# Optimization experiments

Hardware: AMD Instinct MI355X
Metric: run time of the kernel (lower is better)

The kernel has to match this reference:

```python
import jax, jax.numpy as jnp
import numpy as np

B, N_MAX, D_MODEL, K_F, ROD_ID_DIM = 16384, 64, 256, 8, 8
BETA = 10000.0
PRECOMP = 64  # FourierFeatures precompute_limit
DISK_FEAT = 2 + 2 * K_F + 3 + ROD_ID_DIM   # 29
ROD_FEAT = 2 + 1 + 1 + 2 * 2 * K_F + ROD_ID_DIM  # 44


def fourier_table():
    # sin/cos interleaved as in torch: stack([sin,cos],-1).view(P, 2K)
    k = jnp.arange(K_F, dtype=jnp.float32)
    omega = BETA ** (-2.0 * k / (2.0 * K_F))
    idx = jnp.arange(PRECOMP, dtype=jnp.float32)
    oi = idx[:, None] * omega  # (P, K)
    return jnp.stack([jnp.sin(oi), jnp.cos(oi)], axis=-1).reshape(PRECOMP, 2 * K_F)


def setup_inputs() -> dict:
    key = jax.random.key(0)
    ks = jax.random.split(key, 8)
    state = jax.random.randint(ks[0], (B, N_MAX), 0, 3, dtype=jnp.int32)
    s = 0.02
    return {
        'state': state,
        'rod_id_embed': jax.random.normal(ks[1], (3, ROD_ID_DIM), jnp.float32),
        'disk_W': jax.random.normal(ks[2], (DISK_FEAT, D_MODEL), jnp.float32) * s,
        'disk_b': jax.random.normal(ks[3], (D_MODEL,), jnp.float32) * s,
        'rod_W': jax.random.normal(ks[4], (ROD_FEAT, D_MODEL), jnp.float32) * s,
        'rod_b': jax.random.normal(ks[5], (D_MODEL,), jnp.float32) * s,
        'null_fourier': jax.random.normal(ks[6], (2 * K_F,), jnp.float32) * s,
        'padding_embedding': jax.random.normal(ks[7], (D_MODEL,), jnp.float32) * s,
    }


def reference(state, rod_id_embed, disk_W, disk_b, rod_W, rod_b, null_fourier, padding_embedding):
    Bq, N = state.shape
    table = fourier_table()                      # (P, 2K)
    valid = state != -1                          # (B, N)
    lengths = valid.sum(axis=1)                  # (B,)
    state_safe = jnp.clip(state, 0, 2)

    # ---- vectorized _compute_state_info ----
    onehot = (state[:, None, :] == jnp.arange(3, dtype=state.dtype)[None, :, None]) & valid[:, None, :]  # (B,3,N)
    oh = onehot.astype(jnp.float32)
    counts = oh.sum(-1)                          # (B,3) disks per rod
    is_empty = counts == 0.0
    len_norm = counts / jnp.maximum(lengths, 1).astype(jnp.float32)[:, None]
    top_disk = jnp.argmax(onehot, axis=-1)       # min index on rod (top = smallest disk)
    bottom_disk = (N - 1) - jnp.argmax(onehot[:, :, ::-1], axis=-1)
    # per-disk: 'above' = # of smaller-index disks on same rod (exclusive prefix sum)
    cum = jnp.cumsum(oh, axis=-1) - oh           # (B,3,N)
    above = jnp.take_along_axis(cum, state_safe[:, None, :], axis=1)[:, 0, :]   # (B,N)
    height = jnp.take_along_axis(counts, state_safe, axis=1)                    # (B,N)
    vf = valid.astype(jnp.float32)
    is_top = (above == 0.0).astype(jnp.float32) * vf
    is_bottom = (above == height - 1.0).astype(jnp.float32) * vf
    depth_norm = jnp.where(height > 1.0, above / jnp.maximum(height - 1.0, 1.0), 0.0) * vf

    # ---- rod nodes (3) ----
    rod_type = jnp.broadcast_to(jnp.array([0.0, 1.0], jnp.float32), (Bq, 3, 2))
    top_f = table[top_disk]                      # (B,3,2K)
    bot_f = table[bottom_disk]
    emp = is_empty[:, :, None]
    top_f = jnp.where(emp, null_fourier, top_f)
    bot_f = jnp.where(emp, null_fourier, bot_f)
    rod_ids = jnp.broadcast_to(rod_id_embed[None], (Bq, 3, ROD_ID_DIM))
    rod_feats = jnp.concatenate([
        rod_type, len_norm[:, :, None], emp.astype(jnp.float32), top_f, bot_f, rod_ids], axis=-1)  # (B,3,44)
    rod_emb = jnp.einsum('brf,fd->brd', rod_feats, rod_W) + rod_b

    # ---- disk nodes (N) ----
    disk_type = jnp.broadcast_to(jnp.array([1.0, 0.0], jnp.float32), (Bq, N, 2))
    size_f = jnp.broadcast_to(table[:N][None], (Bq, N, 2 * K_F))
    rod_id_vec = rod_id_embed[state_safe]        # (B,N,rod_id_dim)
    disk_feats = jnp.concatenate([
        disk_type, size_f, depth_norm[:, :, None], is_top[:, :, None], is_bottom[:, :, None], rod_id_vec], axis=-1)  # (B,N,29)
    disk_emb = jnp.einsum('bnf,fd->bnd', disk_feats, disk_W) + disk_b
    disk_emb = jnp.where(valid[:, :, None], disk_emb, padding_embedding)

    return jnp.concatenate([rod_emb, disk_emb], axis=1)  # (B, 3+N, d_model)
```

## Files before the change

kernel.cpp:

```cpp
#include <hip/hip_runtime.h>

#define DM 256
#define NMAX 64

#define OFF_BASEROD 49152
#define OFF_RODTOP  49920
#define OFF_RODBOT  66560

typedef float vf4 __attribute__((ext_vector_type(4)));

static __device__ __forceinline__ vf4 ld4(const float* p) {
  return *reinterpret_cast<const vf4*>(p);
}
static __device__ __forceinline__ void st4_nt(float* p, vf4 v) {
  __builtin_nontemporal_store(v, reinterpret_cast<vf4*>(p));
}

__global__ void precomp_kernel(
    const float* __restrict__ rod_id_embed,
    const float* __restrict__ disk_W,
    const float* __restrict__ disk_b,
    const float* __restrict__ rod_W,
    const float* __restrict__ rod_b,
    const float* __restrict__ null_fourier,
    float* __restrict__ ws) {
  const int idx = blockIdx.x;
  const int d = threadIdx.x;

  float F[16];
  if (idx < 64) {
#pragma unroll
    for (int k = 0; k < 8; ++k) {
      float omega = powf(10000.0f, -(float)k * 0.125f);
      float a = (float)idx * omega;
      F[2 * k]     = sinf(a);
      F[2 * k + 1] = cosf(a);
    }
  } else {
#pragma unroll
    for (int k = 0; k < 16; ++k) F[k] = null_fourier[k];
  }

  float* bdc     = ws;
  float* baseRod = ws + OFF_BASEROD;
  float* rodTop  = ws + OFF_RODTOP;
  float* rodBot  = ws + OFF_RODBOT;

  float t = 0.f, bo = 0.f;
#pragma unroll
  for (int k = 0; k < 16; ++k) {
    t  += F[k] * rod_W[(4 + k) * DM + d];
    bo += F[k] * rod_W[(20 + k) * DM + d];
  }
  rodTop[idx * DM + d] = t;
  rodBot[idx * DM + d] = bo;

  if (idx < 64) {
    float base = disk_b[d] + disk_W[0 * DM + d];
#pragma unroll
    for (int k = 0; k < 16; ++k) base += F[k] * disk_W[(2 + k) * DM + d];
#pragma unroll
    for (int s = 0; s < 3; ++s) {
      float v = base;
#pragma unroll
      for (int j = 0; j < 8; ++j)
        v += rod_id_embed[s * 8 + j] * disk_W[(21 + j) * DM + d];
      bdc[(size_t)(s * 64 + idx) * DM + d] = v;
    }
  }
  if (idx < 3) {
    float br = rod_b[d] + rod_W[1 * DM + d];
#pragma unroll
    for (int j = 0; j < 8; ++j)
      br += rod_id_embed[idx * 8 + j] * rod_W[(36 + j) * DM + d];
    baseRod[idx * DM + d] = br;
  }
}

__launch_bounds__(256)
__global__ void enc_kernel(
    const int* __restrict__ state,
    const float* __restrict__ disk_W,
    const float* __restrict__ rod_W,
    const float* __restrict__ padding_embedding,
    const float* __restrict__ ws,
    float* __restrict__ out,
    int Btot) {
  const float* bdc     = ws;
  const float* baseRod = ws + OFF_BASEROD;
  const float* rodTop  = ws + OFF_RODTOP;
  const float* rodBot  = ws + OFF_RODBOT;

  const int w    = threadIdx.x >> 6;
  const int lane = threadIdx.x & 63;
  long b = (long)blockIdx.x * 4 + w;
  if (b >= Btot) b = Btot - 1;

  __shared__ vf4 meta_sh[4][64];
  __shared__ float lnorm_sh[4][3];
  __shared__ float emp_sh[4][3];
  __shared__ int   ti_sh[4][3];
  __shared__ int   bi_sh[4][3];

  const int s = state[b * NMAX + lane];
  const bool valid = (s >= 0);
  const int ss = s <= 0 ? 0 : (s >= 2 ? 2 : s);
  const unsigned long long m0 = __ballot(valid && s == 0);
  const unsigned long long m1 = __ballot(valid && s == 1);
  const unsigned long long m2 = __ballot(valid && s == 2);
  const unsigned long long vm = __ballot(valid);
  const unsigned long long mym = (ss == 0) ? m0 : ((ss == 1) ? m1 : m2);
  const int above  = __popcll(mym & ((1ull << lane) - 1ull));
  const int height = __popcll(mym);

  vf4 md;
  md.x = valid ? (float)(ss + 1) : 0.f;
  md.y = (valid && height > 1) ? (float)above / (float)(height - 1) : 0.f;
  md.z = (valid && above == 0) ? 1.f : 0.f;
  md.w = (valid && above == height - 1) ? 1.f : 0.f;
  meta_sh[w][lane] = md;

  if (lane < 3) {
    const unsigned long long m = (lane == 0) ? m0 : ((lane == 1) ? m1 : m2);
    const int cnt = __popcll(m);
    const int lengths = __popcll(vm);
    lnorm_sh[w][lane] = (float)cnt / (float)(lengths > 1 ? lengths : 1);
    emp_sh[w][lane]   = (cnt == 0) ? 1.f : 0.f;
    ti_sh[w][lane]    = cnt ? (int)__builtin_ctzll(m) : 64;
    bi_sh[w][lane]    = cnt ? 63 - (int)__builtin_clzll(m) : 64;
  }
  __syncthreads();

  const int c0 = lane * 4;
  const vf4 Wdep = ld4(disk_W + 18 * DM + c0);
  const vf4 Wt   = ld4(disk_W + 19 * DM + c0);
  const vf4 Wb   = ld4(disk_W + 20 * DM + c0);
  const vf4 pad  = ld4(padding_embedding + c0);
  const vf4 rW2  = ld4(rod_W + 2 * DM + c0);
  const vf4 rW3  = ld4(rod_W + 3 * DM + c0);

  float* outB = out + (size_t)b * 67 * DM;

#pragma unroll
  for (int r = 0; r < 3; ++r) {
    const float ln = lnorm_sh[w][r];
    const float em = emp_sh[w][r];
    const int ti = ti_sh[w][r];
    const int bi = bi_sh[w][r];
    vf4 v = ld4(baseRod + r * DM + c0);
    const vf4 tf = ld4(rodTop + (size_t)ti * DM + c0);
    const vf4 bf = ld4(rodBot + (size_t)bi * DM + c0);
    v += ln * rW2 + em * rW3 + tf + bf;
    st4_nt(outB + r * DM + c0, v);
  }

#pragma unroll 8
  for (int i = 0; i < 64; ++i) {
    const vf4 md2 = meta_sh[w][i];
    vf4 v;
    if (md2.x > 0.5f) {
      const int c = (int)md2.x - 1;
      const vf4 base = ld4(bdc + (size_t)(c * 64 + i) * DM + c0);
      v = base + md2.y * Wdep + md2.z * Wt + md2.w * Wb;
    } else {
      v = pad;
    }
    st4_nt(outB + (size_t)(3 + i) * DM + c0, v);
  }
}

extern "C" void kernel_launch(void* const* d_in, const int* in_sizes, int n_in,
                              void* d_out, int out_size, void* d_ws, size_t ws_size,
                              hipStream_t stream) {
  const int*   state             = (const int*)d_in[0];
  const float* rod_id_embed      = (const float*)d_in[1];
  const float* disk_W            = (const float*)d_in[2];
  const float* disk_b            = (const float*)d_in[3];
  const float* rod_W             = (const float*)d_in[4];
  const float* rod_b             = (const float*)d_in[5];
  const float* null_fourier      = (const float*)d_in[6];
  const float* padding_embedding = (const float*)d_in[7];
  float* ws  = (float*)d_ws;
  float* out = (float*)d_out;

  const int B = in_sizes[0] / NMAX;

  hipLaunchKernelGGL(precomp_kernel, dim3(65), dim3(256), 0, stream,
                     rod_id_embed, disk_W, disk_b, rod_W, rod_b, null_fourier, ws);
  hipLaunchKernelGGL(enc_kernel, dim3((B + 3) / 4), dim3(256), 0, stream,
                     state, disk_W, rod_W, padding_embedding, ws, out, B);
}
```

Before: 228.5 us.

## Stage per-disk base table in LDS and split out rod-id projection

The precompute step now stores one 64x256 disk base table plus a separate 3x256 rod-id projection, replacing the earlier three per-rod copies. Each encoder block loads the 64 KB base table into shared memory and adds the selected rod-id projection from registers, instead of gathering from a 192-row global table. Blocks grow to 512 threads covering 8 batch rows, which spreads the staging cost over more rows. The 64 KB of LDS per block limits occupancy and adds a global-to-LDS copy per block, while the kernel is largely bound by output stores.

Result: faster. 223.4 us (-2.2%).

```diff
diff --git a/kernel.cpp b/kernel.cpp
--- a/kernel.cpp
+++ b/kernel.cpp
@@ -3,9 +3,10 @@
 #define DM 256
 #define NMAX 64
 
-#define OFF_BASEROD 49152
-#define OFF_RODTOP  49920
-#define OFF_RODBOT  66560
+#define OFF_RIDPROJ 16384
+#define OFF_BASEROD 17152
+#define OFF_RODTOP  17920
+#define OFF_RODBOT  34560
 
 typedef float vf4 __attribute__((ext_vector_type(4)));
 
@@ -41,10 +42,11 @@
     for (int k = 0; k < 16; ++k) F[k] = null_fourier[k];
   }
 
-  float* bdc     = ws;
-  float* baseRod = ws + OFF_BASEROD;
-  float* rodTop  = ws + OFF_RODTOP;
-  float* rodBot  = ws + OFF_RODBOT;
+  float* baseDisk = ws;
+  float* ridproj  = ws + OFF_RIDPROJ;
+  float* baseRod  = ws + OFF_BASEROD;
+  float* rodTop   = ws + OFF_RODTOP;
+  float* rodBot   = ws + OFF_RODBOT;
 
   float t = 0.f, bo = 0.f;
 #pragma unroll
@@ -59,25 +61,24 @@
     float base = disk_b[d] + disk_W[0 * DM + d];
 #pragma unroll
     for (int k = 0; k < 16; ++k) base += F[k] * disk_W[(2 + k) * DM + d];
-#pragma unroll
-    for (int s = 0; s < 3; ++s) {
-      float v = base;
-#pragma unroll
-      for (int j = 0; j < 8; ++j)
-        v += rod_id_embed[s * 8 + j] * disk_W[(21 + j) * DM + d];
-      bdc[(size_t)(s * 64 + idx) * DM + d] = v;
+    baseDisk[(size_t)idx * DM + d] = base;
+  }
+  if (idx < 3) {
+    float rp = 0.f;
+    float br = rod_b[d] + rod_W[1 * DM + d];
+#pragma unroll
+    for (int j = 0; j < 8; ++j) {
+      rp += rod_id_embed[idx * 8 + j] * disk_W[(21 + j) * DM + d];
+      br += rod_id_embed[idx * 8 + j] * rod_W[(36 + j) * DM + d];
     }
-  }
-  if (idx < 3) {
-    float br = rod_b[d] + rod_W[1 * DM + d];
-#pragma unroll
-    for (int j = 0; j < 8; ++j)
-      br += rod_id_embed[idx * 8 + j] * rod_W[(36 + j) * DM + d];
+    ridproj[idx * DM + d] = rp;
     baseRod[idx * DM + d] = br;
   }
 }
 
-__launch_bounds__(256)
+#define BLK_B 8
+
+__launch_bounds__(512)
 __global__ void enc_kernel(
     const int* __restrict__ state,
     const float* __restrict__ disk_W,
@@ -86,21 +87,30 @@
     const float* __restrict__ ws,
     float* __restrict__ out,
     int Btot) {
-  const float* bdc     = ws;
-  const float* baseRod = ws + OFF_BASEROD;
-  const float* rodTop  = ws + OFF_RODTOP;
-  const float* rodBot  = ws + OFF_RODBOT;
-
-  const int w    = threadIdx.x >> 6;
-  const int lane = threadIdx.x & 63;
-  long b = (long)blockIdx.x * 4 + w;
+  const float* baseDisk = ws;
+  const float* ridproj  = ws + OFF_RIDPROJ;
+  const float* baseRod  = ws + OFF_BASEROD;
+  const float* rodTop   = ws + OFF_RODTOP;
+  const float* rodBot   = ws + OFF_RODBOT;
+
+  const int tid  = threadIdx.x;
+  const int w    = tid >> 6;
+  const int lane = tid & 63;
+  long b = (long)blockIdx.x * BLK_B + w;
   if (b >= Btot) b = Btot - 1;
 
-  __shared__ vf4 meta_sh[4][64];
-  __shared__ float lnorm_sh[4][3];
-  __shared__ float emp_sh[4][3];
-  __shared__ int   ti_sh[4][3];
-  __shared__ int   bi_sh[4][3];
+  __shared__ float base_sh[64 * DM];
+  __shared__ vf4  meta_sh[BLK_B][64];
+  __shared__ float lnorm_sh[BLK_B][3];
+  __shared__ float emp_sh[BLK_B][3];
+  __shared__ int   ti_sh[BLK_B][3];
+  __shared__ int   bi_sh[BLK_B][3];
+
+#pragma unroll
+  for (int k = 0; k < 8; ++k) {
+    const int i4 = tid + k * 512;
+    *(reinterpret_cast<vf4*>(base_sh) + i4) = ld4(baseDisk + (size_t)i4 * 4);
+  }
 
   const int s = state[b * NMAX + lane];
   const bool valid = (s >= 0);
@@ -138,6 +148,9 @@
   const vf4 pad  = ld4(padding_embedding + c0);
   const vf4 rW2  = ld4(rod_W + 2 * DM + c0);
   const vf4 rW3  = ld4(rod_W + 3 * DM + c0);
+  const vf4 rp0  = ld4(ridproj + 0 * DM + c0);
+  const vf4 rp1  = ld4(ridproj + 1 * DM + c0);
+  const vf4 rp2  = ld4(ridproj + 2 * DM + c0);
 
   float* outB = out + (size_t)b * 67 * DM;
 
@@ -159,9 +172,9 @@
     const vf4 md2 = meta_sh[w][i];
     vf4 v;
     if (md2.x > 0.5f) {
-      const int c = (int)md2.x - 1;
-      const vf4 base = ld4(bdc + (size_t)(c * 64 + i) * DM + c0);
-      v = base + md2.y * Wdep + md2.z * Wt + md2.w * Wb;
+      const vf4 base = ld4(base_sh + i * DM + c0);
+      const vf4 rp = (md2.x < 1.5f) ? rp0 : ((md2.x < 2.5f) ? rp1 : rp2);
+      v = base + rp + md2.y * Wdep + md2.z * Wt + md2.w * Wb;
     } else {
       v = pad;
     }
@@ -187,6 +200,6 @@
 
   hipLaunchKernelGGL(precomp_kernel, dim3(65), dim3(256), 0, stream,
                      rod_id_embed, disk_W, disk_b, rod_W, rod_b, null_fourier, ws);
-  hipLaunchKernelGGL(enc_kernel, dim3((B + 3) / 4), dim3(256), 0, stream,
+  hipLaunchKernelGGL(enc_kernel, dim3((B + BLK_B - 1) / BLK_B), dim3(512), 0, stream,
                      state, disk_W, rod_W, padding_embedding, ws, out, B);
 }
```
